# Performance work log

Hardware: AMD Instinct MI355X
Metric: run time of the kernel (lower is better)

Reference implementation:

```python
import jax, jax.numpy as jnp
import numpy as np

IMG_DIM = 256
AUD_DIM = 256
N_HEADS = 8


def _linear_params(key, fan_in, fan_out):
    k1, k2 = jax.random.split(key)
    lim = 1.0 / np.sqrt(fan_in)
    W = jax.random.uniform(k1, (fan_in, fan_out), minval=-lim, maxval=lim, dtype=jnp.float32)
    b = jax.random.uniform(k2, (fan_out,), minval=-lim, maxval=lim, dtype=jnp.float32)
    return W, b


def setup_inputs() -> dict:
    key = jax.random.key(0)
    ks = jax.random.split(key, 16)
    B, Nv, Na = 16, 1024, 512
    inp = {
        "image_feat": jax.random.normal(ks[0], (B, Nv, IMG_DIM), dtype=jnp.float32),
        "audio_feat": jax.random.normal(ks[1], (B, Na, AUD_DIM), dtype=jnp.float32),
    }
    inp["Wq_i"], inp["bq_i"] = _linear_params(ks[2], IMG_DIM, IMG_DIM)
    inp["Wk_i"], inp["bk_i"] = _linear_params(ks[3], IMG_DIM, IMG_DIM)
    inp["Wv_i"], inp["bv_i"] = _linear_params(ks[4], IMG_DIM, IMG_DIM)
    inp["Wo_i"], inp["bo_i"] = _linear_params(ks[5], AUD_DIM, IMG_DIM)  # out_proj_image
    inp["Wq_a"], inp["bq_a"] = _linear_params(ks[6], AUD_DIM, AUD_DIM)
    inp["Wk_a"], inp["bk_a"] = _linear_params(ks[7], AUD_DIM, AUD_DIM)
    inp["Wv_a"], inp["bv_a"] = _linear_params(ks[8], AUD_DIM, AUD_DIM)
    inp["Wo_a"], inp["bo_a"] = _linear_params(ks[9], IMG_DIM, AUD_DIM)  # out_proj_audio
    inp["Wc1_i"], inp["bc1_i"] = _linear_params(ks[10], IMG_DIM + 2, IMG_DIM)
    inp["Wc2_i"], inp["bc2_i"] = _linear_params(ks[11], IMG_DIM, N_HEADS)
    inp["Wc1_a"], inp["bc1_a"] = _linear_params(ks[12], AUD_DIM + 2, AUD_DIM)
    inp["Wc2_a"], inp["bc2_a"] = _linear_params(ks[13], AUD_DIM, N_HEADS)
    inp["Wg_i"], inp["bg_i"] = _linear_params(ks[14], IMG_DIM, IMG_DIM)
    inp["Wg_a"], inp["bg_a"] = _linear_params(ks[15], AUD_DIM, AUD_DIM)
    return inp


def _heads(x, W, b, H):
    # x: [B, N, C] -> [B, H, N, C//H]
    B, N, _ = x.shape
    y = x @ W + b
    return y.reshape(B, N, H, -1).transpose(0, 2, 1, 3)


def _fwd(image_feat, audio_feat,
         Wq_i, bq_i, Wk_i, bk_i, Wv_i, bv_i, Wo_i, bo_i,
         Wq_a, bq_a, Wk_a, bk_a, Wv_a, bv_a, Wo_a, bo_a,
         Wc1_i, bc1_i, Wc2_i, bc2_i, Wc1_a, bc1_a, Wc2_a, bc2_a,
         Wg_i, bg_i, Wg_a, bg_a):
    H = N_HEADS
    B, Nv, Ci = image_feat.shape
    _, Na, Ca = audio_feat.shape
    scale_img = (Ci // H) ** (-0.5)
    scale_aud = (Ca // H) ** (-0.5)

    tp_img = image_feat.mean(axis=1)  # [B, Ci]
    tp_aud = audio_feat.mean(axis=1)  # [B, Ca]
    spatial_cond = jnp.linalg.norm(image_feat, axis=-1).mean(axis=1, keepdims=True)  # [B,1]
    time_cond = jnp.linalg.norm(audio_feat, axis=-1).mean(axis=1, keepdims=True)     # [B,1]

    # --- audio queries attend over image keys/values ---
    Q_a = _heads(audio_feat, Wq_a, bq_a, H)   # [B,H,Na,d]
    K_i = _heads(image_feat, Wk_i, bk_i, H)   # [B,H,Nv,d]
    V_i = _heads(image_feat, Wv_i, bv_i, H)   # [B,H,Nv,d]
    cond_aud = jnp.concatenate([tp_aud, spatial_cond, time_cond], axis=-1)  # [B,Ca+2]
    bias_a = (jax.nn.relu(cond_aud @ Wc1_a + bc1_a) @ Wc2_a + bc2_a)        # [B,H]
    logits_a = jnp.einsum('bhqd,bhkd->bhqk', Q_a, K_i) * scale_aud + bias_a[:, :, None, None]
    attn_a = jax.nn.softmax(logits_a, axis=-1)
    fused_a = jnp.einsum('bhqk,bhkd->bhqd', attn_a, V_i)  # [B,H,Na,d]
    fused_a = fused_a.transpose(0, 2, 1, 3).reshape(B, Na, Ci)
    fused_a = fused_a @ Wo_a + bo_a                        # [B,Na,Ca]
    gate_a = jax.nn.sigmoid(tp_aud @ Wg_a + bg_a)[:, None, :]
    audio_out = gate_a * fused_a + (1.0 - gate_a) * audio_feat

    # --- image queries attend over UPDATED audio keys/values ---
    Q_i = _heads(image_feat, Wq_i, bq_i, H)   # [B,H,Nv,d]
    K_a = _heads(audio_out, Wk_a, bk_a, H)    # [B,H,Na,d]
    V_a = _heads(audio_out, Wv_a, bv_a, H)    # [B,H,Na,d]
    cond_img = jnp.concatenate([tp_img, spatial_cond, time_cond], axis=-1)  # [B,Ci+2]
    bias_i = (jax.nn.relu(cond_img @ Wc1_i + bc1_i) @ Wc2_i + bc2_i)        # [B,H]
    logits_i = jnp.einsum('bhqd,bhkd->bhqk', Q_i, K_a) * scale_img + bias_i[:, :, None, None]
    attn_i = jax.nn.softmax(logits_i, axis=-1)
    fused_i = jnp.einsum('bhqk,bhkd->bhqd', attn_i, V_a)  # [B,H,Nv,d]
    fused_i = fused_i.transpose(0, 2, 1, 3).reshape(B, Nv, Ca)
    fused_i = fused_i @ Wo_i + bo_i                        # [B,Nv,Ci]
    gate_i = jax.nn.sigmoid(tp_img @ Wg_i + bg_i)[:, None, :]
    image_out = gate_i * fused_i + (1.0 - gate_i) * image_feat

    return image_out, audio_out


def reference(image_feat, audio_feat,
              Wq_i, bq_i, Wk_i, bk_i, Wv_i, bv_i, Wo_i, bo_i,
              Wq_a, bq_a, Wk_a, bk_a, Wv_a, bv_a, Wo_a, bo_a,
              Wc1_i, bc1_i, Wc2_i, bc2_i, Wc1_a, bc1_a, Wc2_a, bc2_a,
              Wg_i, bg_i, Wg_a, bg_a):
    return _fwd(image_feat, audio_feat,
                Wq_i, bq_i, Wk_i, bk_i, Wv_i, bv_i, Wo_i, bo_i,
                Wq_a, bq_a, Wk_a, bk_a, Wv_a, bv_a, Wo_a, bo_a,
                Wc1_i, bc1_i, Wc2_i, bc2_i, Wc1_a, bc1_a, Wc2_a, bc2_a,
                Wg_i, bg_i, Wg_a, bg_a)
```

## Files before the change

### kernel.cpp

```cpp
#include <hip/hip_runtime.h>

#define C 256

typedef short s16x8 __attribute__((ext_vector_type(8)));
typedef float f32x4 __attribute__((ext_vector_type(4)));

#if __has_builtin(__builtin_amdgcn_exp2f)
#define EXP2F __builtin_amdgcn_exp2f
#else
#define EXP2F exp2f
#endif

__device__ __forceinline__ unsigned short f2b(float f) {
    unsigned u = __float_as_uint(f);
    unsigned r = (u + 0x7fffu + ((u >> 16) & 1u)) >> 16;
    return (unsigned short)r;
}

__device__ __forceinline__ unsigned pack2(float a, float b) {
    return __builtin_amdgcn_perm(__float_as_uint(b) + 0x8000u,
                                 __float_as_uint(a) + 0x8000u, 0x07060302u);
}

__global__ void cast_mean_kernel(const float* __restrict__ x, unsigned short* __restrict__ y,
                                 float* __restrict__ part, int N, int nseg) {
    __shared__ float red[4][C];
    int b = blockIdx.x, seg = blockIdx.y;
    int tid = threadIdx.x;
    int cg = tid & 63;
    int rg = tid >> 6;
    int iters = nseg >> 2;
    const float* xp = x + ((size_t)b * N + (size_t)seg * nseg + rg) * C + cg * 4;
    unsigned short* yp = y + ((size_t)b * N + (size_t)seg * nseg + rg) * C + cg * 4;
    float s0 = 0.f, s1 = 0.f, s2 = 0.f, s3 = 0.f;
    for (int i = 0; i < iters; ++i) {
        float4 v = *(const float4*)(xp + (size_t)i * 4 * C);
        s0 += v.x; s1 += v.y; s2 += v.z; s3 += v.w;
        ushort4 o; o.x = f2b(v.x); o.y = f2b(v.y); o.z = f2b(v.z); o.w = f2b(v.w);
        *(ushort4*)(yp + (size_t)i * 4 * C) = o;
    }
    float4 s4 = {s0, s1, s2, s3};
    *(float4*)&red[rg][cg * 4] = s4;
    __syncthreads();
    float s = red[0][tid] + red[1][tid] + red[2][tid] + red[3][tid];
    part[(b * 8 + seg) * C + tid] = s;
}

struct WPtrs { const float* src[8]; unsigned short* dst[8]; };
__global__ void wtrans_kernel(WPtrs p) {
    const float* W = p.src[blockIdx.y];
    unsigned short* Wt = p.dst[blockIdx.y];
    int n = blockIdx.x * 64 + (threadIdx.x & 63);
    int k0 = (threadIdx.x >> 6) * 64;
#pragma unroll
    for (int kk = 0; kk < 64; kk += 4) {
        float a0 = W[(size_t)(k0 + kk + 0) * C + n];
        float a1 = W[(size_t)(k0 + kk + 1) * C + n];
        float a2 = W[(size_t)(k0 + kk + 2) * C + n];
        float a3 = W[(size_t)(k0 + kk + 3) * C + n];
        ushort4 o; o.x = f2b(a0); o.y = f2b(a1); o.z = f2b(a2); o.w = f2b(a3);
        *(ushort4*)(Wt + (size_t)n * C + k0 + kk) = o;
    }
}

__global__ void gate_kernel(const float* __restrict__ partI, const float* __restrict__ partA,
                            const float* __restrict__ WgI, const float* __restrict__ WgA,
                            const float* __restrict__ bgI, const float* __restrict__ bgA,
                            float* __restrict__ gI, float* __restrict__ gA,
                            float invNv, float invNa) {
    __shared__ float t[C];
    int b = blockIdx.x, c = threadIdx.x;
    const float* part = blockIdx.y ? partA : partI;
    const float* Wg = blockIdx.y ? WgA : WgI;
    const float* bg = blockIdx.y ? bgA : bgI;
    float* g = blockIdx.y ? gA : gI;
    float invN = blockIdx.y ? invNa : invNv;
    float s = 0.f;
#pragma unroll
    for (int j = 0; j < 8; ++j) s += part[(b * 8 + j) * C + c];
    t[c] = s * invN;
    __syncthreads();
    float acc = bg[c];
#pragma unroll 8
    for (int k = 0; k < C; ++k) acc += t[k] * Wg[k * C + c];
    g[b * C + c] = 1.f / (1.f + __expf(-acc));
}

template <bool BIAS_ON_M, bool GATED, bool STORE_BF16, bool STORE_F32>
__global__ __launch_bounds__(256, 2) void gemm16(
    const unsigned short* __restrict__ A, const unsigned short* __restrict__ Bt,
    const float* __restrict__ bias, float* __restrict__ Yf, unsigned short* __restrict__ Yh,
    int M, int N, const float* __restrict__ gate, const float* __restrict__ resid,
    int rows_per_b, float oscale) {
    __shared__ unsigned short sA[128 * 40];
    __shared__ unsigned short sB[64 * 40];
    const int tid = threadIdx.x;
    const int wave = tid >> 6, lane = tid & 63;
    const int quad = lane >> 4, l16 = lane & 15;
    const int bm = blockIdx.y * 128, bn = blockIdx.x * 64;

    const int ar0 = (tid) >> 2, ac0 = tid & 3;
    const int ar1 = (tid + 256) >> 2;
    const int br = tid >> 2, bc = tid & 3;

    f32x4 acc[2][4];
#pragma unroll
    for (int i = 0; i < 2; ++i)
#pragma unroll
        for (int j = 0; j < 4; ++j) acc[i][j] = (f32x4){0.f, 0.f, 0.f, 0.f};

    uint4 pa0 = *(const uint4*)(A + (size_t)(bm + ar0) * 256 + ac0 * 8);
    uint4 pa1 = *(const uint4*)(A + (size_t)(bm + ar1) * 256 + ac0 * 8);
    uint4 pb  = *(const uint4*)(Bt + (size_t)(bn + br) * 256 + bc * 8);

    for (int k0 = 0; k0 < 256; k0 += 32) {
        __syncthreads();
        *(uint4*)(sA + ar0 * 40 + ac0 * 8) = pa0;
        *(uint4*)(sA + ar1 * 40 + ac0 * 8) = pa1;
        *(uint4*)(sB + br * 40 + bc * 8) = pb;
        if (k0 < 224) {
            pa0 = *(const uint4*)(A + (size_t)(bm + ar0) * 256 + k0 + 32 + ac0 * 8);
            pa1 = *(const uint4*)(A + (size_t)(bm + ar1) * 256 + k0 + 32 + ac0 * 8);
            pb  = *(const uint4*)(Bt + (size_t)(bn + br) * 256 + k0 + 32 + bc * 8);
        }
        __syncthreads();
        s16x8 af[2], bf[4];
#pragma unroll
        for (int mt = 0; mt < 2; ++mt)
            af[mt] = *(const s16x8*)(sA + (wave * 32 + mt * 16 + l16) * 40 + quad * 8);
#pragma unroll
        for (int nt = 0; nt < 4; ++nt)
            bf[nt] = *(const s16x8*)(sB + (nt * 16 + l16) * 40 + quad * 8);
#pragma unroll
        for (int mt = 0; mt < 2; ++mt)
#pragma unroll
            for (int nt = 0; nt < 4; ++nt)
                acc[mt][nt] = __builtin_amdgcn_mfma_f32_16x16x32_bf16(af[mt], bf[nt], acc[mt][nt], 0, 0, 0);
    }

    const int b = GATED ? (bm / rows_per_b) : 0;
#pragma unroll
    for (int mt = 0; mt < 2; ++mt) {
#pragma unroll
        for (int nt = 0; nt < 4; ++nt) {
            int n = bn + nt * 16 + l16;
            float bias_n = BIAS_ON_M ? 0.f : bias[n];
            float g = GATED ? gate[b * C + n] : 0.f;
#pragma unroll
            for (int r = 0; r < 4; ++r) {
                int m = bm + wave * 32 + mt * 16 + quad * 4 + r;
                float y = acc[mt][nt][r] + (BIAS_ON_M ? bias[m] : bias_n);
                if (GATED) {
                    float rv = resid[(size_t)m * C + n];
                    y = g * y + (1.f - g) * rv;
                }
                if (STORE_F32) Yf[(size_t)m * N + n] = y;
                if (STORE_BF16) Yh[(size_t)m * N + n] = f2b(y * oscale);
            }
        }
    }
}

__global__ __launch_bounds__(256) void attn_mfma(
    const unsigned short* __restrict__ Q, const unsigned short* __restrict__ K,
    const unsigned short* __restrict__ Vt, unsigned short* __restrict__ O,
    int Nq, int Nk, int vtStride) {
    __shared__ unsigned short sK[64 * 40];
    __shared__ unsigned short sVt[32 * 72];
    __shared__ unsigned short sP[4][16 * 40];
    const int tid = threadIdx.x;
    const int wave = tid >> 6, lane = tid & 63;
    const int quad = lane >> 4, l16 = lane & 15;
    const int b = blockIdx.z, h = blockIdx.y;
    const int q0 = blockIdx.x * 64 + wave * 16;

    s16x8 qf = *(const s16x8*)(Q + ((size_t)b * Nq + q0 + l16) * 256 + h * 32 + quad * 8);
    f32x4 oacc[2];
    oacc[0] = (f32x4){0.f, 0.f, 0.f, 0.f};
    oacc[1] = (f32x4){0.f, 0.f, 0.f, 0.f};
    float rs = 0.f;

    const int kr = tid >> 2, kc = tid & 3;
    const int vr = tid >> 3, vc = tid & 7;
    const unsigned short* Kb = K + (size_t)b * Nk * 256 + h * 32;
    const unsigned short* Vb = Vt + (size_t)(h * 32 + vr) * vtStride + (size_t)b * Nk;

    uint4 kreg = *(const uint4*)(Kb + (size_t)kr * 256 + kc * 8);
    uint4 vreg = *(const uint4*)(Vb + vc * 8);

    for (int k0 = 0; k0 < Nk; k0 += 64) {
        __syncthreads();
        *(uint4*)(sK + kr * 40 + kc * 8) = kreg;
        *(uint4*)(sVt + vr * 72 + vc * 8) = vreg;
        if (k0 + 64 < Nk) {
            kreg = *(const uint4*)(Kb + (size_t)(k0 + 64 + kr) * 256 + kc * 8);
            vreg = *(const uint4*)(Vb + k0 + 64 + vc * 8);
        }
        __syncthreads();
        unsigned short* p = &sP[wave][0];
#pragma unroll
        for (int kg = 0; kg < 2; ++kg) {
#pragma unroll
            for (int kt = 0; kt < 2; ++kt) {
                s16x8 kf = *(const s16x8*)(sK + (kg * 32 + kt * 16 + l16) * 40 + quad * 8);
                f32x4 z = (f32x4){0.f, 0.f, 0.f, 0.f};
                f32x4 st = __builtin_amdgcn_mfma_f32_16x16x32_bf16(kf, qf, z, 0, 0, 0);
                float p0 = EXP2F(st[0]), p1 = EXP2F(st[1]);
                float p2 = EXP2F(st[2]), p3 = EXP2F(st[3]);
                rs += (p0 + p1) + (p2 + p3);
                uint2 pk;
                pk.x = pack2(p0, p1);
                pk.y = pack2(p2, p3);
                *(uint2*)(p + l16 * 40 + kt * 16 + quad * 4) = pk;
            }
            s16x8 pf = *(const s16x8*)(p + l16 * 40 + quad * 8);
#pragma unroll
            for (int dh = 0; dh < 2; ++dh) {
                s16x8 vf = *(const s16x8*)(sVt + (dh * 16 + l16) * 72 + kg * 32 + quad * 8);
                oacc[dh] = __builtin_amdgcn_mfma_f32_16x16x32_bf16(pf, vf, oacc[dh], 0, 0, 0);
            }
        }
    }

    rs += __shfl_xor(rs, 16, 64);
    rs += __shfl_xor(rs, 32, 64);
    float inv = 1.f / rs;
    float invq[4];
#pragma unroll
    for (int r = 0; r < 4; ++r) invq[r] = __shfl(inv, quad * 4 + r, 64);
#pragma unroll
    for (int dh = 0; dh < 2; ++dh)
#pragma unroll
        for (int r = 0; r < 4; ++r)
            O[((size_t)b * Nq + q0 + quad * 4 + r) * 256 + h * 32 + dh * 16 + l16] =
                f2b(oacc[dh][r] * invq[r]);
}

extern "C" void kernel_launch(void* const* d_in, const int* in_sizes, int n_in,
                              void* d_out, int out_size, void* d_ws, size_t ws_size,
                              hipStream_t stream) {
    (void)in_sizes; (void)n_in; (void)out_size; (void)ws_size;
    const float* img  = (const float*)d_in[0];
    const float* aud  = (const float*)d_in[1];
    const float* Wq_i = (const float*)d_in[2];  const float* bq_i = (const float*)d_in[3];
    const float* Wk_i = (const float*)d_in[4];  const float* bk_i = (const float*)d_in[5];
    const float* Wv_i = (const float*)d_in[6];  const float* bv_i = (const float*)d_in[7];
    const float* Wo_i = (const float*)d_in[8];  const float* bo_i = (const float*)d_in[9];
    const float* Wq_a = (const float*)d_in[10]; const float* bq_a = (const float*)d_in[11];
    const float* Wk_a = (const float*)d_in[12]; const float* bk_a = (const float*)d_in[13];
    const float* Wv_a = (const float*)d_in[14]; const float* bv_a = (const float*)d_in[15];
    const float* Wo_a = (const float*)d_in[16]; const float* bo_a = (const float*)d_in[17];
    const float* Wg_i = (const float*)d_in[26]; const float* bg_i = (const float*)d_in[27];
    const float* Wg_a = (const float*)d_in[28]; const float* bg_a = (const float*)d_in[29];

    const int B = 16, Nv = 1024, Na = 512;
    const int Mi = B * Nv, Ma = B * Na;
    const size_t MiC = (size_t)Mi * C;
    const size_t MaC = (size_t)Ma * C;

    float* out_img = (float*)d_out;
    float* out_aud = out_img + MiC;

    unsigned short* wsu = (unsigned short*)d_ws;
    unsigned short* R1 = wsu;
    unsigned short* R2 = R1 + MiC;
    unsigned short* R3 = R2 + MiC;
    unsigned short* R4 = R3 + MiC;
    unsigned short* R5 = R4 + MaC;
    unsigned short* R6 = R5 + MaC;
    unsigned short* R7 = R6 + MaC;
    unsigned short* wt = R7 + MaC;
    float* fws   = (float*)(wt + 8 * 65536);
    float* partI = fws;
    float* partA = partI + B * 8 * C;
    float* gI    = partA + B * 8 * C;
    float* gA    = gI + B * C;

    unsigned short* wtQa = wt + 0 * 65536;
    unsigned short* wtKi = wt + 1 * 65536;
    unsigned short* wtVi = wt + 2 * 65536;
    unsigned short* wtOa = wt + 3 * 65536;
    unsigned short* wtKa = wt + 4 * 65536;
    unsigned short* wtVa = wt + 5 * 65536;
    unsigned short* wtQi = wt + 6 * 65536;
    unsigned short* wtOi = wt + 7 * 65536;

    const float qs = 0.17677669529663687f * 1.4426950408889634f;
    dim3 blk(256);

    cast_mean_kernel<<<dim3(B, 8), blk, 0, stream>>>(img, R1, partI, Nv, Nv / 8);
    cast_mean_kernel<<<dim3(B, 8), blk, 0, stream>>>(aud, R4, partA, Na, Na / 8);
    WPtrs wp;
    wp.src[0] = Wq_a; wp.dst[0] = wtQa;
    wp.src[1] = Wk_i; wp.dst[1] = wtKi;
    wp.src[2] = Wv_i; wp.dst[2] = wtVi;
    wp.src[3] = Wo_a; wp.dst[3] = wtOa;
    wp.src[4] = Wk_a; wp.dst[4] = wtKa;
    wp.src[5] = Wv_a; wp.dst[5] = wtVa;
    wp.src[6] = Wq_i; wp.dst[6] = wtQi;
    wp.src[7] = Wo_i; wp.dst[7] = wtOi;
    wtrans_kernel<<<dim3(4, 8), blk, 0, stream>>>(wp);
    gate_kernel<<<dim3(B, 2), C, 0, stream>>>(partI, partA, Wg_i, Wg_a, bg_i, bg_a,
                                              gI, gA, 1.f / Nv, 1.f / Na);

    gemm16<false, false, true, false><<<dim3(4, Ma / 128), blk, 0, stream>>>(
        R4, wtQa, bq_a, nullptr, R5, Ma, 256, nullptr, nullptr, 0, qs);
    gemm16<false, false, true, false><<<dim3(4, Mi / 128), blk, 0, stream>>>(
        R1, wtKi, bk_i, nullptr, R2, Mi, 256, nullptr, nullptr, 0, 1.f);
    gemm16<true, false, true, false><<<dim3(Mi / 64, 2), blk, 0, stream>>>(
        wtVi, R1, bv_i, nullptr, R3, 256, Mi, nullptr, nullptr, 0, 1.f);
    attn_mfma<<<dim3(Na / 64, 8, B), blk, 0, stream>>>(R5, R2, R3, R6, Na, Nv, Mi);
    gemm16<false, true, true, true><<<dim3(4, Ma / 128), blk, 0, stream>>>(
        R6, wtOa, bo_a, out_aud, R7, Ma, 256, gA, aud, Na, 1.f);

    gemm16<false, false, true, false><<<dim3(4, Ma / 128), blk, 0, stream>>>(
        R7, wtKa, bk_a, nullptr, R5, Ma, 256, nullptr, nullptr, 0, 1.f);
    gemm16<true, false, true, false><<<dim3(Ma / 64, 2), blk, 0, stream>>>(
        wtVa, R7, bv_a, nullptr, R6, 256, Ma, nullptr, nullptr, 0, 1.f);
    gemm16<false, false, true, false><<<dim3(4, Mi / 128), blk, 0, stream>>>(
        R1, wtQi, bq_i, nullptr, R3, Mi, 256, nullptr, nullptr, 0, qs);
    attn_mfma<<<dim3(Nv / 64, 8, B), blk, 0, stream>>>(R3, R5, R6, R2, Nv, Na, Ma);
    gemm16<false, true, false, true><<<dim3(4, Mi / 128), blk, 0, stream>>>(
        R2, wtOi, bo_i, out_img, nullptr, Mi, 256, gI, img, Nv, 1.f);
}
```

Before: 263.8 us.

## Merge prep and projection GEMMs into grouped launches, restructure attention to register K/V

```diff
diff --git a/kernel.cpp b/kernel.cpp
--- a/kernel.cpp
+++ b/kernel.cpp
@@ -22,13 +22,13 @@
                                  __float_as_uint(a) + 0x8000u, 0x07060302u);
 }
 
-__global__ void cast_mean_kernel(const float* __restrict__ x, unsigned short* __restrict__ y,
-                                 float* __restrict__ part, int N, int nseg) {
+struct WPtrs { const float* src[8]; unsigned short* dst[8]; };
+
+__device__ __forceinline__ void cast_mean_body(
+    const float* __restrict__ x, unsigned short* __restrict__ y, float* __restrict__ part,
+    int N, int nseg, int b, int seg, int tid) {
     __shared__ float red[4][C];
-    int b = blockIdx.x, seg = blockIdx.y;
-    int tid = threadIdx.x;
-    int cg = tid & 63;
-    int rg = tid >> 6;
+    int cg = tid & 63, rg = tid >> 6;
     int iters = nseg >> 2;
     const float* xp = x + ((size_t)b * N + (size_t)seg * nseg + rg) * C + cg * 4;
     unsigned short* yp = y + ((size_t)b * N + (size_t)seg * nseg + rg) * C + cg * 4;
@@ -46,60 +46,157 @@
     part[(b * 8 + seg) * C + tid] = s;
 }
 
-struct WPtrs { const float* src[8]; unsigned short* dst[8]; };
-__global__ void wtrans_kernel(WPtrs p) {
-    const float* W = p.src[blockIdx.y];
-    unsigned short* Wt = p.dst[blockIdx.y];
-    int n = blockIdx.x * 64 + (threadIdx.x & 63);
-    int k0 = (threadIdx.x >> 6) * 64;
-#pragma unroll
-    for (int kk = 0; kk < 64; kk += 4) {
-        float a0 = W[(size_t)(k0 + kk + 0) * C + n];
-        float a1 = W[(size_t)(k0 + kk + 1) * C + n];
-        float a2 = W[(size_t)(k0 + kk + 2) * C + n];
-        float a3 = W[(size_t)(k0 + kk + 3) * C + n];
-        ushort4 o; o.x = f2b(a0); o.y = f2b(a1); o.z = f2b(a2); o.w = f2b(a3);
-        *(ushort4*)(Wt + (size_t)n * C + k0 + kk) = o;
-    }
-}
-
-__global__ void gate_kernel(const float* __restrict__ partI, const float* __restrict__ partA,
-                            const float* __restrict__ WgI, const float* __restrict__ WgA,
-                            const float* __restrict__ bgI, const float* __restrict__ bgA,
-                            float* __restrict__ gI, float* __restrict__ gA,
-                            float invNv, float invNa) {
-    __shared__ float t[C];
-    int b = blockIdx.x, c = threadIdx.x;
-    const float* part = blockIdx.y ? partA : partI;
-    const float* Wg = blockIdx.y ? WgA : WgI;
-    const float* bg = blockIdx.y ? bgA : bgI;
-    float* g = blockIdx.y ? gA : gI;
-    float invN = blockIdx.y ? invNa : invNv;
-    float s = 0.f;
-#pragma unroll
-    for (int j = 0; j < 8; ++j) s += part[(b * 8 + j) * C + c];
-    t[c] = s * invN;
-    __syncthreads();
-    float acc = bg[c];
+__global__ void prep_kernel(const float* __restrict__ img, const float* __restrict__ aud,
+                            unsigned short* __restrict__ R1, unsigned short* __restrict__ R4,
+                            float* __restrict__ partI, float* __restrict__ partA, WPtrs wp) {
+    int x = blockIdx.x, tid = threadIdx.x;
+    if (x < 128) {
+        cast_mean_body(img, R1, partI, 1024, 128, x >> 3, x & 7, tid);
+    } else if (x < 256) {
+        int id = x - 128;
+        cast_mean_body(aud, R4, partA, 512, 64, id >> 3, id & 7, tid);
+    } else {
+        int id = x - 256;
+        const float* W = wp.src[id >> 2];
+        unsigned short* Wt = wp.dst[id >> 2];
+        int n = (id & 3) * 64 + (tid & 63);
+        int k0 = (tid >> 6) * 64;
+#pragma unroll
+        for (int kk = 0; kk < 64; kk += 4) {
+            float a0 = W[(size_t)(k0 + kk + 0) * C + n];
+            float a1 = W[(size_t)(k0 + kk + 1) * C + n];
+            float a2 = W[(size_t)(k0 + kk + 2) * C + n];
+            float a3 = W[(size_t)(k0 + kk + 3) * C + n];
+            ushort4 o; o.x = f2b(a0); o.y = f2b(a1); o.z = f2b(a2); o.w = f2b(a3);
+            *(ushort4*)(Wt + (size_t)n * C + k0 + kk) = o;
+        }
+    }
+}
+
+struct GDesc {
+    const unsigned short* A;
+    const unsigned short* Bt;
+    const float* bias;
+    unsigned short* Yh;
+    int N;
+    int start;
+    int lnb;
+    int bias_on_m;
+    float oscale;
+};
+struct GArgs {
+    GDesc d[4];
+    int off1, off2, off3;
+    int gemm_total;
+    const float* partI; const float* partA;
+    const float* WgI; const float* WgA;
+    const float* bgI; const float* bgA;
+    float* gI; float* gA;
+    float invNv, invNa;
+};
+
+__global__ __launch_bounds__(256, 2) void gemm_multi(GArgs ga) {
+    __shared__ unsigned short sA[128 * 40];
+    __shared__ unsigned short sB[64 * 40];
+    const int bid = blockIdx.x;
+    const int tid = threadIdx.x;
+
+    if (bid >= ga.gemm_total) {
+        float* t = (float*)sA;
+        int id = bid - ga.gemm_total;
+        int b = id >> 1, which = id & 1;
+        const float* part = which ? ga.partA : ga.partI;
+        const float* Wg = which ? ga.WgA : ga.WgI;
+        const float* bg = which ? ga.bgA : ga.bgI;
+        float* g = which ? ga.gA : ga.gI;
+        float invN = which ? ga.invNa : ga.invNv;
+        float s = 0.f;
+#pragma unroll
+        for (int j = 0; j < 8; ++j) s += part[(b * 8 + j) * C + tid];
+        t[tid] = s * invN;
+        __syncthreads();
+        float acc = bg[tid];
 #pragma unroll 8
-    for (int k = 0; k < C; ++k) acc += t[k] * Wg[k * C + c];
-    g[b * C + c] = 1.f / (1.f + __expf(-acc));
-}
-
-template <bool BIAS_ON_M, bool GATED, bool STORE_BF16, bool STORE_F32>
-__global__ __launch_bounds__(256, 2) void gemm16(
+        for (int k = 0; k < C; ++k) acc += t[k] * Wg[k * C + tid];
+        g[b * C + tid] = 1.f / (1.f + __expf(-acc));
+        return;
+    }
+
+    const int j = (bid >= ga.off1) + (bid >= ga.off2) + (bid >= ga.off3);
+    const GDesc d = ga.d[j];
+    const int local = bid - d.start;
+    const int bn = (local & ((1 << d.lnb) - 1)) * 64;
+    const int bm = (local >> d.lnb) * 128;
+
+    const int wave = tid >> 6, lane = tid & 63;
+    const int quad = lane >> 4, l16 = lane & 15;
+    const int ar0 = tid >> 2, ac0 = tid & 3;
+    const int ar1 = (tid + 256) >> 2;
+    const int br = tid >> 2, bc = tid & 3;
+
+    f32x4 acc[2][4];
+#pragma unroll
+    for (int i = 0; i < 2; ++i)
+#pragma unroll
+        for (int k = 0; k < 4; ++k) acc[i][k] = (f32x4){0.f, 0.f, 0.f, 0.f};
+
+    uint4 pa0 = *(const uint4*)(d.A + (size_t)(bm + ar0) * 256 + ac0 * 8);
+    uint4 pa1 = *(const uint4*)(d.A + (size_t)(bm + ar1) * 256 + ac0 * 8);
+    uint4 pb  = *(const uint4*)(d.Bt + (size_t)(bn + br) * 256 + bc * 8);
+
+    for (int k0 = 0; k0 < 256; k0 += 32) {
+        __syncthreads();
+        *(uint4*)(sA + ar0 * 40 + ac0 * 8) = pa0;
+        *(uint4*)(sA + ar1 * 40 + ac0 * 8) = pa1;
+        *(uint4*)(sB + br * 40 + bc * 8) = pb;
+        if (k0 < 224) {
+            pa0 = *(const uint4*)(d.A + (size_t)(bm + ar0) * 256 + k0 + 32 + ac0 * 8);
+            pa1 = *(const uint4*)(d.A + (size_t)(bm + ar1) * 256 + k0 + 32 + ac0 * 8);
+            pb  = *(const uint4*)(d.Bt + (size_t)(bn + br) * 256 + k0 + 32 + bc * 8);
+        }
+        __syncthreads();
+        s16x8 af[2], bf[4];
+#pragma unroll
+        for (int mt = 0; mt < 2; ++mt)
+            af[mt] = *(const s16x8*)(sA + (wave * 32 + mt * 16 + l16) * 40 + quad * 8);
+#pragma unroll
+        for (int nt = 0; nt < 4; ++nt)
+            bf[nt] = *(const s16x8*)(sB + (nt * 16 + l16) * 40 + quad * 8);
+#pragma unroll
+        for (int mt = 0; mt < 2; ++mt)
+#pragma unroll
+            for (int nt = 0; nt < 4; ++nt)
+                acc[mt][nt] = __builtin_amdgcn_mfma_f32_16x16x32_bf16(af[mt], bf[nt], acc[mt][nt], 0, 0, 0);
+    }
+
+#pragma unroll
+    for (int mt = 0; mt < 2; ++mt) {
+#pragma unroll
+        for (int nt = 0; nt < 4; ++nt) {
+            int n = bn + nt * 16 + l16;
+            float bias_n = d.bias_on_m ? 0.f : d.bias[n];
+#pragma unroll
+            for (int r = 0; r < 4; ++r) {
+                int m = bm + wave * 32 + mt * 16 + quad * 4 + r;
+                float y = acc[mt][nt][r] + (d.bias_on_m ? d.bias[m] : bias_n);
+                d.Yh[(size_t)m * d.N + n] = f2b(y * d.oscale);
+            }
+        }
+    }
+}
+
+template <bool STORE_BF16>
+__global__ __launch_bounds__(256, 2) void gemm_out(
     const unsigned short* __restrict__ A, const unsigned short* __restrict__ Bt,
     const float* __restrict__ bias, float* __restrict__ Yf, unsigned short* __restrict__ Yh,
-    int M, int N, const float* __restrict__ gate, const float* __restrict__ resid,
-    int rows_per_b, float oscale) {
+    int M, const float* __restrict__ gate, const float* __restrict__ resid, int rows_per_b) {
     __shared__ unsigned short sA[128 * 40];
     __shared__ unsigned short sB[64 * 40];
     const int tid = threadIdx.x;
     const int wave = tid >> 6, lane = tid & 63;
     const int quad = lane >> 4, l16 = lane & 15;
     const int bm = blockIdx.y * 128, bn = blockIdx.x * 64;
-
-    const int ar0 = (tid) >> 2, ac0 = tid & 3;
+    const int ar0 = tid >> 2, ac0 = tid & 3;
     const int ar1 = (tid + 256) >> 2;
     const int br = tid >> 2, bc = tid & 3;
 
@@ -107,7 +204,7 @@
 #pragma unroll
     for (int i = 0; i < 2; ++i)
 #pragma unroll
-        for (int j = 0; j < 4; ++j) acc[i][j] = (f32x4){0.f, 0.f, 0.f, 0.f};
+        for (int k = 0; k < 4; ++k) acc[i][k] = (f32x4){0.f, 0.f, 0.f, 0.f};
 
     uint4 pa0 = *(const uint4*)(A + (size_t)(bm + ar0) * 256 + ac0 * 8);
     uint4 pa1 = *(const uint4*)(A + (size_t)(bm + ar1) * 256 + ac0 * 8);
@@ -138,24 +235,22 @@
                 acc[mt][nt] = __builtin_amdgcn_mfma_f32_16x16x32_bf16(af[mt], bf[nt], acc[mt][nt], 0, 0, 0);
     }
 
-    const int b = GATED ? (bm / rows_per_b) : 0;
+    const int b = bm / rows_per_b;
 #pragma unroll
     for (int mt = 0; mt < 2; ++mt) {
 #pragma unroll
         for (int nt = 0; nt < 4; ++nt) {
             int n = bn + nt * 16 + l16;
-            float bias_n = BIAS_ON_M ? 0.f : bias[n];
-            float g = GATED ? gate[b * C + n] : 0.f;
+            float bias_n = bias[n];
+            float g = gate[b * C + n];
 #pragma unroll
             for (int r = 0; r < 4; ++r) {
                 int m = bm + wave * 32 + mt * 16 + quad * 4 + r;
-                float y = acc[mt][nt][r] + (BIAS_ON_M ? bias[m] : bias_n);
-                if (GATED) {
-                    float rv = resid[(size_t)m * C + n];
-                    y = g * y + (1.f - g) * rv;
-                }
-                if (STORE_F32) Yf[(size_t)m * N + n] = y;
-                if (STORE_BF16) Yh[(size_t)m * N + n] = f2b(y * oscale);
+                float y = acc[mt][nt][r] + bias_n;
+                float rv = resid[(size_t)m * C + n];
+                y = g * y + (1.f - g) * rv;
+                Yf[(size_t)m * C + n] = y;
+                if (STORE_BF16) Yh[(size_t)m * C + n] = f2b(y);
             }
         }
     }
@@ -165,75 +260,89 @@
     const unsigned short* __restrict__ Q, const unsigned short* __restrict__ K,
     const unsigned short* __restrict__ Vt, unsigned short* __restrict__ O,
     int Nq, int Nk, int vtStride) {
-    __shared__ unsigned short sK[64 * 40];
-    __shared__ unsigned short sVt[32 * 72];
-    __shared__ unsigned short sP[4][16 * 40];
+    __shared__ unsigned short sP[4][2][16 * 40];
     const int tid = threadIdx.x;
     const int wave = tid >> 6, lane = tid & 63;
     const int quad = lane >> 4, l16 = lane & 15;
     const int b = blockIdx.z, h = blockIdx.y;
-    const int q0 = blockIdx.x * 64 + wave * 16;
-
-    s16x8 qf = *(const s16x8*)(Q + ((size_t)b * Nq + q0 + l16) * 256 + h * 32 + quad * 8);
-    f32x4 oacc[2];
-    oacc[0] = (f32x4){0.f, 0.f, 0.f, 0.f};
-    oacc[1] = (f32x4){0.f, 0.f, 0.f, 0.f};
-    float rs = 0.f;
-
-    const int kr = tid >> 2, kc = tid & 3;
-    const int vr = tid >> 3, vc = tid & 7;
-    const unsigned short* Kb = K + (size_t)b * Nk * 256 + h * 32;
-    const unsigned short* Vb = Vt + (size_t)(h * 32 + vr) * vtStride + (size_t)b * Nk;
-
-    uint4 kreg = *(const uint4*)(Kb + (size_t)kr * 256 + kc * 8);
-    uint4 vreg = *(const uint4*)(Vb + vc * 8);
+    const int q0 = blockIdx.x * 128 + wave * 32;
+
+    s16x8 qf[2];
+    qf[0] = *(const s16x8*)(Q + ((size_t)b * Nq + q0 + l16) * 256 + h * 32 + quad * 8);
+    qf[1] = *(const s16x8*)(Q + ((size_t)b * Nq + q0 + 16 + l16) * 256 + h * 32 + quad * 8);
+    f32x4 oacc[2][2];
+#pragma unroll
+    for (int i = 0; i < 2; ++i)
+#pragma unroll
+        for (int k = 0; k < 2; ++k) oacc[i][k] = (f32x4){0.f, 0.f, 0.f, 0.f};
+    float rs[2] = {0.f, 0.f};
+
+    const unsigned short* Kf = K + ((size_t)b * Nk + l16) * 256 + h * 32 + quad * 8;
+    const unsigned short* Vf0 = Vt + (size_t)(h * 32 + l16) * vtStride + (size_t)b * Nk + quad * 8;
+    const unsigned short* Vf1 = Vf0 + (size_t)16 * vtStride;
+
+    s16x8 kr[4], vr[4];
+#pragma unroll
+    for (int t = 0; t < 4; ++t) kr[t] = *(const s16x8*)(Kf + (size_t)t * 16 * 256);
+    vr[0] = *(const s16x8*)(Vf0);
+    vr[1] = *(const s16x8*)(Vf0 + 32);
+    vr[2] = *(const s16x8*)(Vf1);
+    vr[3] = *(const s16x8*)(Vf1 + 32);
 
     for (int k0 = 0; k0 < Nk; k0 += 64) {
-        __syncthreads();
-        *(uint4*)(sK + kr * 40 + kc * 8) = kreg;
-        *(uint4*)(sVt + vr * 72 + vc * 8) = vreg;
-        if (k0 + 64 < Nk) {
-            kreg = *(const uint4*)(Kb + (size_t)(k0 + 64 + kr) * 256 + kc * 8);
-            vreg = *(const uint4*)(Vb + k0 + 64 + vc * 8);
-        }
-        __syncthreads();
-        unsigned short* p = &sP[wave][0];
+        const int kp = (k0 + 64 < Nk) ? k0 + 64 : k0;
+        s16x8 kn[4], vn[4];
+#pragma unroll
+        for (int t = 0; t < 4; ++t) kn[t] = *(const s16x8*)(Kf + (size_t)(kp + t * 16) * 256);
+        vn[0] = *(const s16x8*)(Vf0 + kp);
+        vn[1] = *(const s16x8*)(Vf0 + kp + 32);
+        vn[2] = *(const s16x8*)(Vf1 + kp);
+        vn[3] = *(const s16x8*)(Vf1 + kp + 32);
+
 #pragma unroll
         for (int kg = 0; kg < 2; ++kg) {
 #pragma unroll
-            for (int kt = 0; kt < 2; ++kt) {
-                s16x8 kf = *(const s16x8*)(sK + (kg * 32 + kt * 16 + l16) * 40 + quad * 8);
-                f32x4 z = (f32x4){0.f, 0.f, 0.f, 0.f};
-                f32x4 st = __builtin_amdgcn_mfma_f32_16x16x32_bf16(kf, qf, z, 0, 0, 0);
-                float p0 = EXP2F(st[0]), p1 = EXP2F(st[1]);
-                float p2 = EXP2F(st[2]), p3 = EXP2F(st[3]);
-                rs += (p0 + p1) + (p2 + p3);
-                uint2 pk;
-                pk.x = pack2(p0, p1);
-                pk.y = pack2(p2, p3);
-                *(uint2*)(p + l16 * 40 + kt * 16 + quad * 4) = pk;
+            for (int q2 = 0; q2 < 2; ++q2) {
+                unsigned short* p = &sP[wave][q2][0];
+#pragma unroll
+                for (int kt = 0; kt < 2; ++kt) {
+                    f32x4 z = (f32x4){0.f, 0.f, 0.f, 0.f};
+                    f32x4 st = __builtin_amdgcn_mfma_f32_16x16x32_bf16(kr[kg * 2 + kt], qf[q2], z, 0, 0, 0);
+                    float p0 = EXP2F(st[0]), p1 = EXP2F(st[1]);
+                    float p2 = EXP2F(st[2]), p3 = EXP2F(st[3]);
+                    rs[q2] += (p0 + p1) + (p2 + p3);
+                    uint2 pk;
+                    pk.x = pack2(p0, p1);
+                    pk.y = pack2(p2, p3);
+                    *(uint2*)(p + l16 * 40 + kt * 16 + quad * 4) = pk;
+                }
             }
-            s16x8 pf = *(const s16x8*)(p + l16 * 40 + quad * 8);
-#pragma unroll
-            for (int dh = 0; dh < 2; ++dh) {
-                s16x8 vf = *(const s16x8*)(sVt + (dh * 16 + l16) * 72 + kg * 32 + quad * 8);
-                oacc[dh] = __builtin_amdgcn_mfma_f32_16x16x32_bf16(pf, vf, oacc[dh], 0, 0, 0);
+#pragma unroll
+            for (int q2 = 0; q2 < 2; ++q2) {
+                s16x8 pf = *(const s16x8*)(&sP[wave][q2][0] + l16 * 40 + quad * 8);
+                oacc[q2][0] = __builtin_amdgcn_mfma_f32_16x16x32_bf16(pf, vr[kg], oacc[q2][0], 0, 0, 0);
+                oacc[q2][1] = __builtin_amdgcn_mfma_f32_16x16x32_bf16(pf, vr[2 + kg], oacc[q2][1], 0, 0, 0);
             }
         }
-    }
-
-    rs += __shfl_xor(rs, 16, 64);
-    rs += __shfl_xor(rs, 32, 64);
-    float inv = 1.f / rs;
-    float invq[4];
-#pragma unroll
-    for (int r = 0; r < 4; ++r) invq[r] = __shfl(inv, quad * 4 + r, 64);
-#pragma unroll
-    for (int dh = 0; dh < 2; ++dh)
-#pragma unroll
-        for (int r = 0; r < 4; ++r)
-            O[((size_t)b * Nq + q0 + quad * 4 + r) * 256 + h * 32 + dh * 16 + l16] =
-                f2b(oacc[dh][r] * invq[r]);
+#pragma unroll
+        for (int t = 0; t < 4; ++t) { kr[t] = kn[t]; vr[t] = vn[t]; }
+    }
+
+#pragma unroll
+    for (int q2 = 0; q2 < 2; ++q2) {
+        float r = rs[q2];
+        r += __shfl_xor(r, 16, 64);
+        r += __shfl_xor(r, 32, 64);
+        float inv = 1.f / r;
+#pragma unroll
+        for (int rr = 0; rr < 4; ++rr) {
+            float iq = __shfl(inv, quad * 4 + rr, 64);
+#pragma unroll
+            for (int dh = 0; dh < 2; ++dh)
+                O[((size_t)b * Nq + q0 + q2 * 16 + quad * 4 + rr) * 256 + h * 32 + dh * 16 + l16] =
+                    f2b(oacc[q2][dh][rr] * iq);
+        }
+    }
 }
 
 extern "C" void kernel_launch(void* const* d_in, const int* in_sizes, int n_in,
@@ -265,7 +374,8 @@
     unsigned short* R1 = wsu;
     unsigned short* R2 = R1 + MiC;
     unsigned short* R3 = R2 + MiC;
-    unsigned short* R4 = R3 + MiC;
+    unsigned short* R8 = R3 + MiC;
+    unsigned short* R4 = R8 + MiC;
     unsigned short* R5 = R4 + MaC;
     unsigned short* R6 = R5 + MaC;
     unsigned short* R7 = R6 + MaC;
@@ -288,8 +398,6 @@
     const float qs = 0.17677669529663687f * 1.4426950408889634f;
     dim3 blk(256);
 
-    cast_mean_kernel<<<dim3(B, 8), blk, 0, stream>>>(img, R1, partI, Nv, Nv / 8);
-    cast_mean_kernel<<<dim3(B, 8), blk, 0, stream>>>(aud, R4, partA, Na, Na / 8);
     WPtrs wp;
     wp.src[0] = Wq_a; wp.dst[0] = wtQa;
     wp.src[1] = Wk_i; wp.dst[1] = wtKi;
@@ -299,27 +407,30 @@
     wp.src[5] = Wv_a; wp.dst[5] = wtVa;
     wp.src[6] = Wq_i; wp.dst[6] = wtQi;
     wp.src[7] = Wo_i; wp.dst[7] = wtOi;
-    wtrans_kernel<<<dim3(4, 8), blk, 0, stream>>>(wp);
-    gate_kernel<<<dim3(B, 2), C, 0, stream>>>(partI, partA, Wg_i, Wg_a, bg_i, bg_a,
-                                              gI, gA, 1.f / Nv, 1.f / Na);
-
-    gemm16<false, false, true, false><<<dim3(4, Ma / 128), blk, 0, stream>>>(
-        R4, wtQa, bq_a, nullptr, R5, Ma, 256, nullptr, nullptr, 0, qs);
-    gemm16<false, false, true, false><<<dim3(4, Mi / 128), blk, 0, stream>>>(
-        R1, wtKi, bk_i, nullptr, R2, Mi, 256, nullptr, nullptr, 0, 1.f);
-    gemm16<true, false, true, false><<<dim3(Mi / 64, 2), blk, 0, stream>>>(
-        wtVi, R1, bv_i, nullptr, R3, 256, Mi, nullptr, nullptr, 0, 1.f);
-    attn_mfma<<<dim3(Na / 64, 8, B), blk, 0, stream>>>(R5, R2, R3, R6, Na, Nv, Mi);
-    gemm16<false, true, true, true><<<dim3(4, Ma / 128), blk, 0, stream>>>(
-        R6, wtOa, bo_a, out_aud, R7, Ma, 256, gA, aud, Na, 1.f);
-
-    gemm16<false, false, true, false><<<dim3(4, Ma / 128), blk, 0, stream>>>(
-        R7, wtKa, bk_a, nullptr, R5, Ma, 256, nullptr, nullptr, 0, 1.f);
-    gemm16<true, false, true, false><<<dim3(Ma / 64, 2), blk, 0, stream>>>(
-        wtVa, R7, bv_a, nullptr, R6, 256, Ma, nullptr, nullptr, 0, 1.f);
-    gemm16<false, false, true, false><<<dim3(4, Mi / 128), blk, 0, stream>>>(
-        R1, wtQi, bq_i, nullptr, R3, Mi, 256, nullptr, nullptr, 0, qs);
-    attn_mfma<<<dim3(Nv / 64, 8, B), blk, 0, stream>>>(R3, R5, R6, R2, Nv, Na, Ma);
-    gemm16<false, true, false, true><<<dim3(4, Mi / 128), blk, 0, stream>>>(
-        R2, wtOi, bo_i, out_img, nullptr, Mi, 256, gI, img, Nv, 1.f);
-}
+    prep_kernel<<<288, blk, 0, stream>>>(img, aud, R1, R4, partI, partA, wp);
+
+    GArgs g1 = {};
+    g1.d[0] = {R4,   wtQa, bq_a, R5, 256,   0,    2, 0, qs };
+    g1.d[1] = {R1,   wtKi, bk_i, R2, 256,   256,  2, 0, 1.f};
+    g1.d[2] = {wtVi, R1,   bv_i, R3, 16384, 768,  8, 1, 1.f};
+    g1.d[3] = {R1,   wtQi, bq_i, R8, 256,   1280, 2, 0, qs };
+    g1.off1 = 256; g1.off2 = 768; g1.off3 = 1280; g1.gemm_total = 1792;
+    g1.partI = partI; g1.partA = partA;
+    g1.WgI = Wg_i; g1.WgA = Wg_a; g1.bgI = bg_i; g1.bgA = bg_a;
+    g1.gI = gI; g1.gA = gA; g1.invNv = 1.f / Nv; g1.invNa = 1.f / Na;
+    gemm_multi<<<1792 + 32, blk, 0, stream>>>(g1);
+
+    attn_mfma<<<dim3(Na / 128, 8, B), blk, 0, stream>>>(R5, R2, R3, R6, Na, Nv, Mi);
+
+    gemm_out<true><<<dim3(4, Ma / 128), blk, 0, stream>>>(R6, wtOa, bo_a, out_aud, R7, Ma, gA, aud, Na);
+
+    GArgs g2 = {};
+    g2.d[0] = {R7,   wtKa, bk_a, R5, 256,  0,   2, 0, 1.f};
+    g2.d[1] = {wtVa, R7,   bv_a, R6, 8192, 256, 7, 1, 1.f};
+    g2.off1 = 256; g2.off2 = 512; g2.off3 = 512; g2.gemm_total = 512;
+    gemm_multi<<<512, blk, 0, stream>>>(g2);
+
+    attn_mfma<<<dim3(Nv / 128, 8, B), blk, 0, stream>>>(R8, R5, R6, R2, Nv, Na, Ma);
+
+    gemm_out<false><<<dim3(4, Mi / 128), blk, 0, stream>>>(R2, wtOi, bo_i, out_img, nullptr, Mi, gI, img, Nv);
+}
```

New measurement: 280.2 us. +6.2%, slower.
